# Performance work log

Measured on AMD Instinct MI355X. Metric: run time of the kernel, lower is better.

The kernel has to match this reference:

```python
import jax, jax.numpy as jnp
import numpy as np

IN_FEATURES = 4096
OUT_FEATURES = 4096
N_TOKENS = 8192  # flattened batch*seq


def setup_inputs() -> dict:
    key = jax.random.key(0)
    kx, kw = jax.random.split(key)
    x = jax.random.normal(kx, (N_TOKENS, IN_FEATURES), dtype=jnp.float16)
    # Full weight [out, in], split into a 2:4 structured part and the complement
    # (mirrors prune_2_to_4's [0,0,1,1] pattern along the in dim).
    W = jax.random.normal(kw, (OUT_FEATURES, IN_FEATURES), dtype=jnp.float16)
    pattern = jnp.asarray([0, 0, 1, 1], dtype=jnp.float16)
    mask = jnp.tile(pattern, IN_FEATURES // 4)  # [in]
    W_dense = W * mask          # 2:4 semi-structured component
    W_sparse = W * (1 - mask)   # unstructured CSR component (complement)
    return {"x": x, "W_dense": W_dense, "W_sparse": W_sparse}


def reference(x, W_dense, W_sparse):
    # Original: out_dense = W_semi @ x^T ; out_sparse = spmm(W_csr, x^T)
    #           out = out_sparse^T + out_dense^T
    # Equivalent: x @ W_dense^T + x @ W_sparse^T, two separate GEMMs summed.
    out_dense = jnp.einsum('ni,oi->no', x, W_dense)
    out_sparse = jnp.einsum('ni,oi->no', x, W_sparse)
    return out_dense + out_sparse
```

## Files before the change

kernel.cpp:

```cpp
#include <hip/hip_runtime.h>
#include <stdint.h>


#define NT 8192
#define NO 4096
#define NK 4096

typedef float f32x4 __attribute__((ext_vector_type(4)));
typedef _Float16 f16x8 __attribute__((ext_vector_type(8)));

__device__ __forceinline__ void gload_lds16(const void* g, void* l) {
  __builtin_amdgcn_global_load_lds(
      (const __attribute__((address_space(1))) void*)g,
      (__attribute__((address_space(3))) void*)l, 16, 0, 0);
}

#define BAR() __builtin_amdgcn_s_barrier()
#define WV6() asm volatile("s_waitcnt vmcnt(6)" ::: "memory")
#define PRIO1() __builtin_amdgcn_s_setprio(1)
#define PRIO0() __builtin_amdgcn_s_setprio(0)

__global__ __launch_bounds__(256) void cvt_all(
    const float* __restrict__ x, const float* __restrict__ wd,
    const float* __restrict__ ws, _Float16* __restrict__ xh,
    _Float16* __restrict__ wh, int nx8, int nw8) {
  int i = blockIdx.x * 256 + threadIdx.x;
  if (i < nx8) {
    const f32x4* p = (const f32x4*)x + 2 * (size_t)i;
    f32x4 lo = p[0], hi = p[1];
    f16x8 r;
#pragma unroll
    for (int j = 0; j < 4; ++j) { r[j] = (_Float16)lo[j]; r[j + 4] = (_Float16)hi[j]; }
    *((f16x8*)xh + i) = r;
  } else {
    int j8 = i - nx8;
    if (j8 < nw8) {
      const f32x4* pd = (const f32x4*)wd + 2 * (size_t)j8;
      const f32x4* ps = (const f32x4*)ws + 2 * (size_t)j8;
      f32x4 dl = pd[0], dh = pd[1], sl = ps[0], sh = ps[1];
      f16x8 r;
#pragma unroll
      for (int j = 0; j < 4; ++j) {
        r[j] = (_Float16)(dl[j] + sl[j]);
        r[j + 4] = (_Float16)(dh[j] + sh[j]);
      }
      *((f16x8*)wh + j8) = r;
    }
  }
}


#define RDA(B_, MG) do { _Pragma("unroll") \
  for (int mm = 0; mm < 4; ++mm) { \
    ar[0][mm] = *(const f16x8*)(Ab[B_] + ((MG)*8 + mm*2 + 0) * 1024 + finner); \
    ar[1][mm] = *(const f16x8*)(Ab[B_] + ((MG)*8 + mm*2 + 1) * 1024 + finner); \
  } } while (0)

#define RDB(B_, NG) do { _Pragma("unroll") \
  for (int nn = 0; nn < 2; ++nn) { \
    br[0][(NG)*2+nn] = *(const f16x8*)(Bb[B_] + ((bsub + (NG)*2 + nn)*2 + 0) * 1024 + finner); \
    br[1][(NG)*2+nn] = *(const f16x8*)(Bb[B_] + ((bsub + (NG)*2 + nn)*2 + 1) * 1024 + finner); \
  } } while (0)

#define MM(MG, NG) do { _Pragma("unroll") \
  for (int ks = 0; ks < 2; ++ks) \
    _Pragma("unroll") for (int mm = 0; mm < 4; ++mm) \
      _Pragma("unroll") for (int nn = 0; nn < 2; ++nn) \
        acc[(MG)*4+mm][(NG)*2+nn] = __builtin_amdgcn_mfma_f32_16x16x32_f16( \
            br[ks][(NG)*2+nn], ar[ks][mm], acc[(MG)*4+mm][(NG)*2+nn], 0, 0, 0); \
  } while (0)

#define STG(BUF_, OP_, H_, S_, KCOL) \
  gload_lds16(((OP_) ? Wrow : Xrow) + ((H_)*128 + (S_)*64) * NK + (KCOL), \
              ldsc + (BUF_)*65536 + (OP_)*32768 + (H_)*16384 + (S_)*8192 + t16)

__global__ __launch_bounds__(512, 2) void gemm8p(
    const _Float16* __restrict__ Xg, const _Float16* __restrict__ Wg,
    float* __restrict__ C) {
  __shared__ _Float16 lds[2][2][2][8192];
  char* ldsc = (char*)&lds[0][0][0][0];

  const int t = threadIdx.x;
  const int lane = t & 63;
  const int wv = t >> 6;
  const int wr = wv >> 2;
  const int wc = wv & 3;
  const int fr = lane & 15;
  const int kq = lane >> 4;
  const int t16 = t * 16;

  const int swz = (blockIdx.x & 7) * 64 + (blockIdx.x >> 3);
  const int bm = swz >> 4, bn = swz & 15;
  const int brow = bm * 256, bcol = bn * 256;

  const int o = t16;
  const int sub = o >> 10;
  const int inner = o & 1023;
  const int innsw = inner ^ (((inner >> 9) & 1) << 5);
  const int rloc = ((sub >> 1) << 4) | ((innsw >> 6) & 15);
  const int kloc = ((sub & 1) << 5) | ((innsw >> 1) & 31);

  const _Float16* Xrow = Xg + (brow + rloc) * NK + kloc;
  const _Float16* Wrow = Wg + (bcol + rloc) * NK + kloc;

  const int finner = ((fr << 6) | (kq << 4)) ^ ((fr & 8) << 2);
  const char* Ab[2] = { ldsc + wr * 16384, ldsc + 65536 + wr * 16384 };
  const char* Bb[2] = { ldsc + 32768 + (wc >> 1) * 16384,
                        ldsc + 65536 + 32768 + (wc >> 1) * 16384 };
  const int bsub = (wc & 1) * 4;

  f16x8 ar[2][4], br[2][4];
  f32x4 acc[8][4] = {};

  STG(0, 0, 0, 0, 0); STG(0, 0, 0, 1, 0); STG(0, 0, 1, 0, 0); STG(0, 0, 1, 1, 0);
  STG(0, 1, 0, 0, 0); STG(0, 1, 0, 1, 0); STG(0, 1, 1, 0, 0); STG(0, 1, 1, 1, 0);
  STG(1, 0, 0, 0, 64); STG(1, 0, 1, 0, 64);
  STG(1, 1, 0, 0, 64); STG(1, 1, 0, 1, 64); STG(1, 1, 1, 0, 64); STG(1, 1, 1, 1, 64);
  WV6(); BAR();

#pragma unroll 1
  for (int i = 0; i < NK / 128; ++i) {
    const int k1 = i * 128 + 64;
    const int kt2 = (i * 128 + 128) & (NK - 1);
    const int kt3 = (i * 128 + 192) & (NK - 1);

    RDA(0, 0); RDB(0, 0); RDB(0, 1);
    STG(1, 0, 0, 1, k1); STG(1, 0, 1, 1, k1);
    PRIO1(); MM(0, 0); MM(0, 1); PRIO0(); BAR();
    RDA(0, 1);
    STG(0, 0, 0, 0, kt2); STG(0, 0, 1, 0, kt2);
    STG(0, 1, 0, 0, kt2); STG(0, 1, 0, 1, kt2);
    STG(0, 1, 1, 0, kt2); STG(0, 1, 1, 1, kt2);
    PRIO1(); MM(1, 0); MM(1, 1); PRIO0();
    WV6(); BAR();

    RDA(1, 0); RDB(1, 0); RDB(1, 1);
    STG(0, 0, 0, 1, kt2); STG(0, 0, 1, 1, kt2);
    PRIO1(); MM(0, 0); MM(0, 1); PRIO0(); BAR();
    RDA(1, 1);
    STG(1, 0, 0, 0, kt3); STG(1, 0, 1, 0, kt3);
    STG(1, 1, 0, 0, kt3); STG(1, 1, 0, 1, kt3);
    STG(1, 1, 1, 0, kt3); STG(1, 1, 1, 1, kt3);
    PRIO1(); MM(1, 0); MM(1, 1); PRIO0();
    WV6(); BAR();
  }

  const long r0 = brow + wr * 128 + fr;
  const int c0 = bcol + wc * 64 + kq * 4;
#pragma unroll
  for (int m = 0; m < 8; ++m)
#pragma unroll
    for (int n = 0; n < 4; ++n)
      *(f32x4*)(C + (r0 + m * 16) * NO + c0 + n * 16) = acc[m][n];
}

__global__ __launch_bounds__(256) void gemm_fb(
    const float* __restrict__ Xf, const float* __restrict__ Wdf,
    const float* __restrict__ Wsf, float* __restrict__ C) {
  __shared__ _Float16 lsA[128 * 32];
  __shared__ _Float16 lsB[128 * 32];

  const int t = threadIdx.x;
  const int lane = t & 63;
  const int wid = t >> 6;
  const int wr = wid >> 1, wc = wid & 1;

  const int nwg = (NT / 128) * (NO / 128);
  const int swz = (blockIdx.x & 7) * (nwg >> 3) + (blockIdx.x >> 3);
  const int nbn = NO / 128;
  const int bm = swz / nbn, bn = swz % nbn;
  const long brow = (long)bm * 128, bcol = (long)bn * 128;

  const int srow = t >> 2;
  const int scol = (t & 3) * 8;
  const float* X  = Xf + (brow + srow) * (long)NK + scol;
  const float* Wd = Wdf + (bcol + srow) * (long)NK + scol;
  const float* Ws = Wsf + (bcol + srow) * (long)NK + scol;
  _Float16* lA = lsA + t * 8;
  _Float16* lB = lsB + t * 8;

  const int fr = lane & 15;
  const int kg = (lane >> 4) * 8;
  const _Float16* pA = lsA + (wr * 64 + fr) * 32 + kg;
  const _Float16* pB = lsB + (wc * 64 + fr) * 32 + kg;

  f32x4 acc[4][4] = {};

  for (int k0 = 0; k0 < NK; k0 += 32) {
    f32x4 aL0 = *(const f32x4*)(X + k0),  aH0 = *(const f32x4*)(X + k0 + 4);
    f32x4 aL1 = *(const f32x4*)(X + k0 + 64 * NK), aH1 = *(const f32x4*)(X + k0 + 64 * NK + 4);
    f32x4 dL0 = *(const f32x4*)(Wd + k0), dH0 = *(const f32x4*)(Wd + k0 + 4);
    f32x4 sL0 = *(const f32x4*)(Ws + k0), sH0 = *(const f32x4*)(Ws + k0 + 4);
    f32x4 dL1 = *(const f32x4*)(Wd + k0 + 64 * NK), dH1 = *(const f32x4*)(Wd + k0 + 64 * NK + 4);
    f32x4 sL1 = *(const f32x4*)(Ws + k0 + 64 * NK), sH1 = *(const f32x4*)(Ws + k0 + 64 * NK + 4);
    __syncthreads();
    f16x8 va0, va1, vb0, vb1;
#pragma unroll
    for (int j = 0; j < 4; ++j) {
      va0[j] = (_Float16)aL0[j];            va0[j + 4] = (_Float16)aH0[j];
      va1[j] = (_Float16)aL1[j];            va1[j + 4] = (_Float16)aH1[j];
      vb0[j] = (_Float16)(dL0[j] + sL0[j]); vb0[j + 4] = (_Float16)(dH0[j] + sH0[j]);
      vb1[j] = (_Float16)(dL1[j] + sL1[j]); vb1[j + 4] = (_Float16)(dH1[j] + sH1[j]);
    }
    *(f16x8*)lA = va0;
    *(f16x8*)(lA + 64 * 32) = va1;
    *(f16x8*)lB = vb0;
    *(f16x8*)(lB + 64 * 32) = vb1;
    __syncthreads();
    f16x8 af[4], bf[4];
#pragma unroll
    for (int i2 = 0; i2 < 4; ++i2) af[i2] = *(const f16x8*)(pA + i2 * 16 * 32);
#pragma unroll
    for (int i2 = 0; i2 < 4; ++i2) bf[i2] = *(const f16x8*)(pB + i2 * 16 * 32);
#pragma unroll
    for (int i2 = 0; i2 < 4; ++i2)
#pragma unroll
      for (int j2 = 0; j2 < 4; ++j2)
        acc[i2][j2] = __builtin_amdgcn_mfma_f32_16x16x32_f16(af[i2], bf[j2], acc[i2][j2], 0, 0, 0);
  }

  const int fq = lane >> 4;
#pragma unroll
  for (int i2 = 0; i2 < 4; ++i2)
#pragma unroll
    for (int j2 = 0; j2 < 4; ++j2)
#pragma unroll
      for (int r = 0; r < 4; ++r) {
        long row = brow + wr * 64 + i2 * 16 + fq * 4 + r;
        long col = bcol + wc * 64 + j2 * 16 + fr;
        C[row * NO + col] = acc[i2][j2][r];
      }
}

extern "C" void kernel_launch(void* const* d_in, const int* in_sizes, int n_in,
                              void* d_out, int out_size, void* d_ws, size_t ws_size,
                              hipStream_t stream) {
  const float* x   = (const float*)d_in[0];
  const float* wd  = (const float*)d_in[1];
  const float* wsp = (const float*)d_in[2];
  float* out = (float*)d_out;

  const size_t xh_bytes = (size_t)NT * NK * 2;
  const size_t wh_bytes = (size_t)NO * NK * 2;

  if (d_ws != nullptr && ws_size >= xh_bytes + wh_bytes) {
    _Float16* xh = (_Float16*)d_ws;
    _Float16* wh = (_Float16*)((char*)d_ws + xh_bytes);
    const int nx8 = NT * NK / 8;
    const int nw8 = NO * NK / 8;
    cvt_all<<<(nx8 + nw8) / 256, 256, 0, stream>>>(x, wd, wsp, xh, wh, nx8, nw8);
    gemm8p<<<(NT / 256) * (NO / 256), 512, 0, stream>>>(xh, wh, out);
  } else {
    gemm_fb<<<(NT / 128) * (NO / 128), 256, 0, stream>>>(x, wd, wsp, out);
  }
}
```

Measured before the change: 302.1 us.

## Ping-pong wave groups so LDS reads and MFMA phases alternate between halves

Splits the 8 waves into two groups by wave row and staggers them. One group issues MFMAs while the other reads fragments from LDS, with barriers between every phase. Global-to-LDS staging is redistributed across the phases and the wait count changes from vmcnt(6) to vmcnt(8). The aim is to keep the matrix units busy continuously while LDS traffic overlaps, at the cost of many more barriers and a more fragile load/wait ordering.

```diff
diff --git a/kernel.cpp b/kernel.cpp
--- a/kernel.cpp
+++ b/kernel.cpp
@@ -16,7 +16,7 @@
 }
 
 #define BAR() __builtin_amdgcn_s_barrier()
-#define WV6() asm volatile("s_waitcnt vmcnt(6)" ::: "memory")
+#define WV8() asm volatile("s_waitcnt vmcnt(8)" ::: "memory")
 #define PRIO1() __builtin_amdgcn_s_setprio(1)
 #define PRIO0() __builtin_amdgcn_s_setprio(0)
 
@@ -62,13 +62,13 @@
     br[1][(NG)*2+nn] = *(const f16x8*)(Bb[B_] + ((bsub + (NG)*2 + nn)*2 + 1) * 1024 + finner); \
   } } while (0)
 
-#define MM(MG, NG) do { _Pragma("unroll") \
+#define MM(MG, NG) do { PRIO1(); _Pragma("unroll") \
   for (int ks = 0; ks < 2; ++ks) \
     _Pragma("unroll") for (int mm = 0; mm < 4; ++mm) \
       _Pragma("unroll") for (int nn = 0; nn < 2; ++nn) \
         acc[(MG)*4+mm][(NG)*2+nn] = __builtin_amdgcn_mfma_f32_16x16x32_f16( \
             br[ks][(NG)*2+nn], ar[ks][mm], acc[(MG)*4+mm][(NG)*2+nn], 0, 0, 0); \
-  } while (0)
+  PRIO0(); } while (0)
 
 #define STG(BUF_, OP_, H_, S_, KCOL) \
   gload_lds16(((OP_) ? Wrow : Xrow) + ((H_)*128 + (S_)*64) * NK + (KCOL), \
@@ -88,6 +88,7 @@
   const int fr = lane & 15;
   const int kq = lane >> 4;
   const int t16 = t * 16;
+  const bool g1 = (wr != 0);
 
   const int swz = (blockIdx.x & 7) * 64 + (blockIdx.x >> 3);
   const int bm = swz >> 4, bn = swz & 15;
@@ -114,35 +115,59 @@
 
   STG(0, 0, 0, 0, 0); STG(0, 0, 0, 1, 0); STG(0, 0, 1, 0, 0); STG(0, 0, 1, 1, 0);
   STG(0, 1, 0, 0, 0); STG(0, 1, 0, 1, 0); STG(0, 1, 1, 0, 0); STG(0, 1, 1, 1, 0);
-  STG(1, 0, 0, 0, 64); STG(1, 0, 1, 0, 64);
+  STG(1, 0, 0, 0, 64); STG(1, 0, 0, 1, 64); STG(1, 0, 1, 0, 64); STG(1, 0, 1, 1, 64);
   STG(1, 1, 0, 0, 64); STG(1, 1, 0, 1, 64); STG(1, 1, 1, 0, 64); STG(1, 1, 1, 1, 64);
-  WV6(); BAR();
+  WV8(); BAR();
+  if (!g1) { RDA(0, 0); RDB(0, 0); }
+  BAR();
 
 #pragma unroll 1
   for (int i = 0; i < NK / 128; ++i) {
-    const int k1 = i * 128 + 64;
     const int kt2 = (i * 128 + 128) & (NK - 1);
     const int kt3 = (i * 128 + 192) & (NK - 1);
 
-    RDA(0, 0); RDB(0, 0); RDB(0, 1);
-    STG(1, 0, 0, 1, k1); STG(1, 0, 1, 1, k1);
-    PRIO1(); MM(0, 0); MM(0, 1); PRIO0(); BAR();
-    RDA(0, 1);
-    STG(0, 0, 0, 0, kt2); STG(0, 0, 1, 0, kt2);
+    if (!g1) { MM(0, 0); } else { RDA(0, 0); RDB(0, 0); }
+    BAR();
+    if (!g1) { RDB(0, 1); } else { MM(0, 0); }
+    BAR();
+    if (!g1) { MM(0, 1); } else { RDB(0, 1); }
+    BAR();
+    if (!g1) { RDA(0, 1); } else { MM(0, 1); }
+    BAR();
     STG(0, 1, 0, 0, kt2); STG(0, 1, 0, 1, kt2);
-    STG(0, 1, 1, 0, kt2); STG(0, 1, 1, 1, kt2);
-    PRIO1(); MM(1, 0); MM(1, 1); PRIO0();
-    WV6(); BAR();
-
-    RDA(1, 0); RDB(1, 0); RDB(1, 1);
-    STG(0, 0, 0, 1, kt2); STG(0, 0, 1, 1, kt2);
-    PRIO1(); MM(0, 0); MM(0, 1); PRIO0(); BAR();
-    RDA(1, 1);
-    STG(1, 0, 0, 0, kt3); STG(1, 0, 1, 0, kt3);
+    if (!g1) { MM(1, 0); } else { RDA(0, 1); }
+    BAR();
+    STG(0, 1, 1, 0, kt2); STG(0, 1, 1, 1, kt2); STG(0, 0, 0, 0, kt2);
+    if (g1) { MM(1, 0); }
+    BAR();
+    STG(0, 0, 0, 1, kt2); STG(0, 0, 1, 0, kt2); STG(0, 0, 1, 1, kt2);
+    if (!g1) { MM(1, 1); }
+    WV8();
+    BAR();
+    if (!g1) { RDA(1, 0); RDB(1, 0); } else { MM(1, 1); }
+    BAR();
+    if (!g1) { MM(0, 0); } else { RDA(1, 0); RDB(1, 0); }
+    BAR();
+    if (!g1) { RDB(1, 1); } else { MM(0, 0); }
+    BAR();
+    if (!g1) { MM(0, 1); } else { RDB(1, 1); }
+    BAR();
     STG(1, 1, 0, 0, kt3); STG(1, 1, 0, 1, kt3);
-    STG(1, 1, 1, 0, kt3); STG(1, 1, 1, 1, kt3);
-    PRIO1(); MM(1, 0); MM(1, 1); PRIO0();
-    WV6(); BAR();
+    if (!g1) { RDA(1, 1); } else { MM(0, 1); }
+    BAR();
+    STG(1, 1, 1, 0, kt3); STG(1, 1, 1, 1, kt3); STG(1, 0, 0, 0, kt3);
+    if (!g1) { MM(1, 0); } else { RDA(1, 1); }
+    BAR();
+    STG(1, 0, 0, 1, kt3); STG(1, 0, 1, 0, kt3);
+    if (g1) { MM(1, 0); }
+    BAR();
+    STG(1, 0, 1, 1, kt3);
+    if (!g1) { MM(1, 1); }
+    WV8();
+    BAR();
+    if (!g1) { RDA(0, 0); RDB(0, 0); }
+    else     { MM(1, 1); }
+    BAR();
   }
 
   const long r0 = brow + wr * 128 + fr;
```

New measurement: 302.5 us. No clear change (+0.1%).
